# Performance work log

Measured on AMD Instinct MI355X. Metric: run time of the kernel, lower is better.

Reference implementation:

```python
import jax, jax.numpy as jnp
import numpy as np

THRESHOLD = 0.5
NEG_POS_RATIO = 3
ALPHA = 1.0
B, A, C, M = 128, 8732, 21, 8


def cxcy_to_xy(c):
    return jnp.concatenate([c[:, :2] - c[:, 2:] / 2.0, c[:, :2] + c[:, 2:] / 2.0], axis=1)


def cxcy_to_gcxgcy(cxcy, priors):
    g_cxcy = (cxcy[:, :2] - priors[:, :2]) / (priors[:, 2:] / 10.0)
    g_wh = jnp.log(cxcy[:, 2:] / priors[:, 2:]) * 5.0
    return jnp.concatenate([g_cxcy, g_wh], axis=1)


def find_jaccard_overlap(a, b):
    # a: [M,4] xy, b: [A,4] xy -> IoU [M,A]
    lt = jnp.maximum(a[:, None, :2], b[None, :, :2])
    rb = jnp.minimum(a[:, None, 2:], b[None, :, 2:])
    wh = jnp.clip(rb - lt, 0.0)
    inter = wh[..., 0] * wh[..., 1]
    area_a = (a[:, 2] - a[:, 0]) * (a[:, 3] - a[:, 1])
    area_b = (b[:, 2] - b[:, 0]) * (b[:, 3] - b[:, 1])
    return inter / (area_a[:, None] + area_b[None, :] - inter)


def setup_inputs() -> dict:
    key = jax.random.key(0)
    k1, k2, k3, k4, k5, k6 = jax.random.split(key, 6)
    predicted_locs = jax.random.normal(k1, (B, A, 4), dtype=jnp.float32)
    predicted_scores = jax.random.normal(k2, (B, A, C), dtype=jnp.float32)
    # ground-truth boxes in xy pixel coords within [0, 300], guaranteed x2>x1, y2>y1
    u = jax.random.uniform(k3, (B, M, 4), dtype=jnp.float32)
    x1y1 = u[..., :2] * 150.0
    x2y2 = x1y1 + u[..., 2:] * 140.0 + 10.0
    boxes = jnp.concatenate([x1y1, x2y2], axis=-1)
    labels = jax.random.randint(k4, (B, M), 1, C)  # 1..20, never background
    # anchor boxes in cxcy, w/h strictly positive
    cxcy = jax.random.uniform(k5, (A, 2), dtype=jnp.float32)
    wh = 0.05 + 0.95 * jax.random.uniform(k6, (A, 2), dtype=jnp.float32)
    anchor_boxes = jnp.concatenate([cxcy, wh], axis=1)
    return {"predicted_locs": predicted_locs, "predicted_scores": predicted_scores,
            "boxes": boxes, "labels": labels, "anchor_boxes": anchor_boxes}


def _match(boxes_i, labels_i, anchors_cxcy, anchors_xy):
    # boxes_i: [M,4] xy pixels, labels_i: [M]
    scaled = boxes_i / 300.0
    iou = find_jaccard_overlap(scaled, anchors_xy)            # [M, A]
    obj_for_anchor = jnp.argmax(iou, axis=0)                  # [A]
    iou_for_anchor = jnp.max(iou, axis=0)                     # [A]
    anchor_for_obj = jnp.argmax(iou, axis=1)                  # [M]
    obj_for_anchor = obj_for_anchor.at[anchor_for_obj].set(jnp.arange(M))
    iou_for_anchor = iou_for_anchor.at[anchor_for_obj].set(1.0)
    label_for_anchor = labels_i[obj_for_anchor]               # [A]
    label_for_anchor = jnp.where(iou_for_anchor < THRESHOLD, 0, label_for_anchor)
    true_locs = cxcy_to_gcxgcy(boxes_i[obj_for_anchor], anchors_cxcy)  # [A,4]
    return label_for_anchor, true_locs


def reference(predicted_locs, predicted_scores, boxes, labels, anchor_boxes):
    anchors_xy = cxcy_to_xy(anchor_boxes)
    true_classes, true_locs = jax.vmap(_match, in_axes=(0, 0, None, None))(
        boxes, labels, anchor_boxes, anchors_xy)              # [B,A], [B,A,4]

    pos = true_classes != 0                                   # [B,A]
    n_pos = pos.sum(axis=1)                                   # [B]
    n_pos_total = n_pos.sum()

    # L1Loss(mean) over positive anchors' 4 coords
    l1 = jnp.abs(predicted_locs - true_locs)                  # [B,A,4]
    loc_loss = (l1 * pos[..., None]).sum() / (n_pos_total.astype(jnp.float32) * 4.0)

    # per-anchor cross entropy
    logp = jax.nn.log_softmax(predicted_scores, axis=-1)      # [B,A,C]
    ce = -jnp.take_along_axis(logp, true_classes[..., None], axis=-1)[..., 0]  # [B,A]

    conf_pos = (ce * pos).sum()
    ce_neg = jnp.where(pos, 0.0, ce)
    ce_neg_sorted = -jnp.sort(-ce_neg, axis=1)                # descending per row
    ranks = jnp.arange(A)[None, :]
    hard = ranks < (NEG_POS_RATIO * n_pos)[:, None]
    conf_hard_neg = (ce_neg_sorted * hard).sum()

    conf_loss = (conf_hard_neg + conf_pos) / n_pos_total.astype(jnp.float32)
    return conf_loss + ALPHA * loc_loss
```

## Files before the change

### kernel.cpp

```cpp
#include <hip/hip_runtime.h>

constexpr int B = 128;
constexpr int A = 8732;
constexpr int C = 21;
constexpr int M = 8;


__global__ __launch_bounds__(1024) void k_match(
    const float* __restrict__ boxes,
    const int*   __restrict__ labels,
    const float* __restrict__ anchors,
    const float* __restrict__ plocs,
    int*         __restrict__ packed,
    int*         __restrict__ row_npos,
    float*       __restrict__ row_loc,
    float*       __restrict__ accf)
{
    __shared__ float         s_iou[A];
    __shared__ unsigned char s_obj[A];
    __shared__ float s_pv[M][16];
    __shared__ int   s_pi[M][16];
    __shared__ int   s_force[M];
    __shared__ int   s_c[16];
    __shared__ float s_l[16];
    __shared__ float s_box[M][4];
    __shared__ int   s_lab[M];

    const int b = blockIdx.x;
    const int t = threadIdx.x;
    const int lane = t & 63;
    const int wv   = t >> 6;

    if (t < M * 4) ((float*)s_box)[t] = boxes[b * M * 4 + t];
    if (t < M)     s_lab[t] = labels[b * M + t];
    __syncthreads();

    float bb[M][4], barea[M];
#pragma unroll
    for (int m = 0; m < M; m++) {
        bb[m][0] = s_box[m][0] / 300.f;
        bb[m][1] = s_box[m][1] / 300.f;
        bb[m][2] = s_box[m][2] / 300.f;
        bb[m][3] = s_box[m][3] / 300.f;
        barea[m] = (bb[m][2] - bb[m][0]) * (bb[m][3] - bb[m][1]);
    }

    float bestv[M];
    int   besti[M];
#pragma unroll
    for (int m = 0; m < M; m++) { bestv[m] = -1.f; besti[m] = 0; }

    const float4* anch4 = (const float4*)anchors;
    for (int a = t; a < A; a += 1024) {
        float4 an = anch4[a];
        float ax1 = an.x - an.z / 2.0f, ay1 = an.y - an.w / 2.0f;
        float ax2 = an.x + an.z / 2.0f, ay2 = an.y + an.w / 2.0f;
        float aarea = (ax2 - ax1) * (ay2 - ay1);

        float bmax = -1.f; int bm = 0;
#pragma unroll
        for (int m = 0; m < M; m++) {
            float lx = fmaxf(bb[m][0], ax1), ly = fmaxf(bb[m][1], ay1);
            float rx = fminf(bb[m][2], ax2), ry = fminf(bb[m][3], ay2);
            float iw = fmaxf(rx - lx, 0.f), ih = fmaxf(ry - ly, 0.f);
            float inter = iw * ih;
            float iou = inter / (barea[m] + aarea - inter);
            if (iou > bmax) { bmax = iou; bm = m; }
            if (iou > bestv[m]) { bestv[m] = iou; besti[m] = a; }
        }
        s_iou[a] = bmax;
        s_obj[a] = (unsigned char)bm;
    }

#pragma unroll
    for (int m = 0; m < M; m++) {
        float v = bestv[m]; int i = besti[m];
        for (int off = 32; off > 0; off >>= 1) {
            float ov = __shfl_down(v, off);
            int   oi = __shfl_down(i, off);
            if (ov > v || (ov == v && oi < i)) { v = ov; i = oi; }
        }
        if (lane == 0) { s_pv[m][wv] = v; s_pi[m][wv] = i; }
    }
    __syncthreads();

    if (t < M) {
        float bv = -1.f; int bi = 0x7fffffff;
#pragma unroll
        for (int w = 0; w < 16; w++) {
            float v = s_pv[t][w]; int i = s_pi[t][w];
            if (v > bv || (v == bv && i < bi)) { bv = v; bi = i; }
        }
        s_force[t] = bi;
    }
    __syncthreads();

    if (t == 0) {
        for (int m = 0; m < M; m++) {
            int a = s_force[m];
            s_obj[a] = (unsigned char)m;
            s_iou[a] = 1.0f;
        }
    }
    __syncthreads();

    int cnt = 0; float lloc = 0.f;
    for (int a = t; a < A; a += 1024) {
        int obj = s_obj[a];
        int lab = (s_iou[a] < 0.5f) ? 0 : s_lab[obj];
        packed[(size_t)b * A + a] = lab;
        if (lab != 0) {
            cnt++;
            float4 an = anch4[a];
            const float* bx = s_box[obj];
            float dx = (bx[0] - an.x) / (an.z / 10.f);
            float dy = (bx[1] - an.y) / (an.w / 10.f);
            float dw = logf(bx[2] / an.z) * 5.f;
            float dh = logf(bx[3] / an.w) * 5.f;
            float4 p = ((const float4*)plocs)[(size_t)b * A + a];
            lloc += fabsf(p.x - dx) + fabsf(p.y - dy) +
                    fabsf(p.z - dw) + fabsf(p.w - dh);
        }
    }
    for (int off = 32; off > 0; off >>= 1) {
        cnt  += __shfl_down(cnt, off);
        lloc += __shfl_down(lloc, off);
    }
    if (lane == 0) { s_c[wv] = cnt; s_l[wv] = lloc; }
    __syncthreads();
    if (t == 0) {
        int tc = 0; float tl = 0.f;
#pragma unroll
        for (int w = 0; w < 16; w++) { tc += s_c[w]; tl += s_l[w]; }
        row_npos[b] = tc;
        row_loc[b]  = tl;
        if (b == 0) accf[0] = 0.f;
    }
}

__global__ __launch_bounds__(256, 4) void k_ce(
    const float* __restrict__ pscores,
    int*         __restrict__ buf,
    float*       __restrict__ accf)
{
    const int tid = blockIdx.x * 256 + threadIdx.x;
    const int q = tid >> 1;
    const int h = tid & 1;
    const float4* sp = (const float4*)pscores + (size_t)q * 21;

    float4 r[11];
    if (h == 0) {
#pragma unroll
        for (int j = 0; j < 11; j++) r[j] = sp[j];
    } else {
#pragma unroll
        for (int j = 0; j < 10; j++) r[j] = sp[11 + j];
    }
    const int4 pk4 = ((const int4*)buf)[q];
    const int labs[4] = {pk4.x, pk4.y, pk4.z, pk4.w};

    float sum[4] = {0.f, 0.f, 0.f, 0.f};
    float sel[4] = {0.f, 0.f, 0.f, 0.f};

    if (h == 0) {
#pragma unroll
        for (int j = 0; j < 11; j++) {
            const float vv[4] = {r[j].x, r[j].y, r[j].z, r[j].w};
#pragma unroll
            for (int e = 0; e < 4; e++) {
                const int fi = j * 4 + e;
                const int al = fi / 21, c = fi % 21;
                sum[al] += __expf(vv[e]);
                if (c == labs[al]) sel[al] = vv[e];
            }
        }
    } else {
#pragma unroll
        for (int j = 0; j < 10; j++) {
            const float vv[4] = {r[j].x, r[j].y, r[j].z, r[j].w};
#pragma unroll
            for (int e = 0; e < 4; e++) {
                const int fi = 44 + j * 4 + e;
                const int al = fi / 21, c = fi % 21;
                sum[al] += __expf(vv[e]);
                if (c == labs[al]) sel[al] = vv[e];
            }
        }
    }
#pragma unroll
    for (int al = 0; al < 4; al++) {
        sum[al] += __shfl_xor(sum[al], 1);
        sel[al] += __shfl_xor(sel[al], 1);
    }

    float l_pos = 0.f;
    if (h == 0) {
        float4 cn;
        float* cnp = (float*)&cn;
#pragma unroll
        for (int al = 0; al < 4; al++) {
            float ce = __logf(sum[al]) - sel[al];
            ce = fmaxf(ce, 0.f);
            if (labs[al] != 0) { l_pos += ce; ce = 0.f; }
            cnp[al] = ce;
        }
        ((float4*)buf)[q] = cn;
    }
    for (int off = 32; off > 0; off >>= 1) l_pos += __shfl_down(l_pos, off);
    if ((threadIdx.x & 63) == 0 && l_pos != 0.f) atomicAdd(&accf[0], l_pos);
}

__global__ __launch_bounds__(1024) void k_topk(
    const float* __restrict__ ce_neg,
    const int*   __restrict__ row_npos,
    float*       __restrict__ row_hard)
{
    __shared__ unsigned vals[A];
    __shared__ unsigned s_u[16];
    __shared__ float    s_f[16];

    const int b = blockIdx.x;
    const int t = threadIdx.x;
    const int lane = t & 63;
    const int wv   = t >> 6;
    const int K = 3 * row_npos[b];
    const float* row = ce_neg + (size_t)b * A;

    {
        const uint4* r4 = (const uint4*)row;
        uint4* v4 = (uint4*)vals;
        for (int i = t; i < A / 4; i += 1024) v4[i] = r4[i];
    }
    __syncthreads();

    if (K <= 0) { if (t == 0) row_hard[b] = 0.f; return; }

    if (K >= A) {
        float s = 0.f;
        for (int i = t; i < A; i += 1024) s += __uint_as_float(vals[i]);
        for (int off = 32; off > 0; off >>= 1) s += __shfl_down(s, off);
        if (lane == 0) s_f[wv] = s;
        __syncthreads();
        if (t == 0) {
            float tot = 0.f;
#pragma unroll
            for (int w = 0; w < 16; w++) tot += s_f[w];
            row_hard[b] = tot;
        }
        return;
    }

    unsigned lo = 0u, hi = 0x7F800000u;
    while (lo < hi) {
        const unsigned mid = lo + ((hi - lo) >> 1);
        int cnt = 0;
        for (int i = t; i < A; i += 1024) cnt += (vals[i] > mid) ? 1 : 0;
        for (int off = 32; off > 0; off >>= 1) cnt += __shfl_down(cnt, off);
        if (lane == 0) s_u[wv] = (unsigned)cnt;
        __syncthreads();
        int tot = 0;
#pragma unroll
        for (int w = 0; w < 16; w++) tot += (int)s_u[w];
        if (tot < K) hi = mid; else lo = mid + 1;
        __syncthreads();
    }
    const unsigned tb = lo;

    float sg = 0.f; int cg = 0;
    for (int i = t; i < A; i += 1024) {
        unsigned v = vals[i];
        if (v > tb) { sg += __uint_as_float(v); cg++; }
    }
    for (int off = 32; off > 0; off >>= 1) {
        sg += __shfl_down(sg, off);
        cg += __shfl_down(cg, off);
    }
    if (lane == 0) { s_f[wv] = sg; s_u[wv] = (unsigned)cg; }
    __syncthreads();
    if (t == 0) {
        float tot = 0.f; int cnt = 0;
#pragma unroll
        for (int w = 0; w < 16; w++) { tot += s_f[w]; cnt += (int)s_u[w]; }
        row_hard[b] = tot + (float)(K - cnt) * __uint_as_float(tb);
    }
}

__global__ __launch_bounds__(128) void k_final(
    const float* __restrict__ accf,
    const int*   __restrict__ row_npos,
    const float* __restrict__ row_loc,
    const float* __restrict__ row_hard,
    float*       __restrict__ out)
{
    __shared__ int   s_n[2];
    __shared__ float s_l[2], s_h[2];
    const int t = threadIdx.x;
    const int lane = t & 63;
    const int wv = t >> 6;

    int np = row_npos[t];
    float lc = row_loc[t];
    float hd = row_hard[t];
    for (int off = 32; off > 0; off >>= 1) {
        np += __shfl_down(np, off);
        lc += __shfl_down(lc, off);
        hd += __shfl_down(hd, off);
    }
    if (lane == 0) { s_n[wv] = np; s_l[wv] = lc; s_h[wv] = hd; }
    __syncthreads();
    if (t == 0) {
        float n = (float)(s_n[0] + s_n[1]);
        float conf = (accf[0] + s_h[0] + s_h[1]) / n;
        float loc  = (s_l[0] + s_l[1]) / (n * 4.f);
        out[0] = conf + loc;
    }
}

extern "C" void kernel_launch(void* const* d_in, const int* in_sizes, int n_in,
                              void* d_out, int out_size, void* d_ws, size_t ws_size,
                              hipStream_t stream)
{
    const float* plocs   = (const float*)d_in[0];
    const float* pscores = (const float*)d_in[1];
    const float* boxes   = (const float*)d_in[2];
    const int*   labels  = (const int*)d_in[3];
    const float* anchors = (const float*)d_in[4];
    float*       out     = (float*)d_out;

    float* accf     = (float*)d_ws;
    int*   row_npos = (int*)d_ws + 8;
    float* row_loc  = (float*)d_ws + 136;
    float* row_hard = (float*)d_ws + 264;
    int*   buf      = (int*)d_ws + 392;

    k_match<<<B, 1024, 0, stream>>>(boxes, labels, anchors, plocs,
                                    buf, row_npos, row_loc, accf);
    k_ce<<<(B * A / 2) / 256, 256, 0, stream>>>(pscores, buf, accf);
    k_topk<<<B, 1024, 0, stream>>>((const float*)buf, row_npos, row_hard);
    k_final<<<1, 128, 0, stream>>>(accf, row_npos, row_loc, row_hard, out);
}
```

Baseline: 292.0 us.

## Stage CE scores through LDS, keep top-k row in registers, fuse final reduce

The cross-entropy kernel becomes a grid-stride loop in which each wave loads 64 anchors' scores with coalesced float4 reads into LDS, and each lane then handles one anchor. The top-k kernel keeps its row in registers instead of LDS, double-buffers the per-wave counts so each bisection step needs one barrier instead of two, and folds the final reduction into the last block through an atomic done counter. This removes one kernel launch and a round of LDS traffic and barriers. The cost is a threadfence/atomic handshake, plus reliance on k_match resetting the counter on every call.

Measured after the change: 319.1 us. +9.3%, slower.

```diff
diff --git a/kernel.cpp b/kernel.cpp
--- a/kernel.cpp
+++ b/kernel.cpp
@@ -14,7 +14,8 @@
     int*         __restrict__ packed,
     int*         __restrict__ row_npos,
     float*       __restrict__ row_loc,
-    float*       __restrict__ accf)
+    float*       __restrict__ accf,
+    int*         __restrict__ done)
 {
     __shared__ float         s_iou[A];
     __shared__ unsigned char s_obj[A];
@@ -134,90 +135,77 @@
         for (int w = 0; w < 16; w++) { tc += s_c[w]; tl += s_l[w]; }
         row_npos[b] = tc;
         row_loc[b]  = tl;
-        if (b == 0) accf[0] = 0.f;
+        if (b == 0) { accf[0] = 0.f; *done = 0; }
     }
 }
 
-__global__ __launch_bounds__(256, 4) void k_ce(
+__global__ __launch_bounds__(256) void k_ce(
     const float* __restrict__ pscores,
     int*         __restrict__ buf,
     float*       __restrict__ accf)
 {
-    const int tid = blockIdx.x * 256 + threadIdx.x;
-    const int q = tid >> 1;
-    const int h = tid & 1;
-    const float4* sp = (const float4*)pscores + (size_t)q * 21;
-
-    float4 r[11];
-    if (h == 0) {
-#pragma unroll
-        for (int j = 0; j < 11; j++) r[j] = sp[j];
-    } else {
-#pragma unroll
-        for (int j = 0; j < 10; j++) r[j] = sp[11 + j];
-    }
-    const int4 pk4 = ((const int4*)buf)[q];
-    const int labs[4] = {pk4.x, pk4.y, pk4.z, pk4.w};
-
-    float sum[4] = {0.f, 0.f, 0.f, 0.f};
-    float sel[4] = {0.f, 0.f, 0.f, 0.f};
-
-    if (h == 0) {
-#pragma unroll
-        for (int j = 0; j < 11; j++) {
-            const float vv[4] = {r[j].x, r[j].y, r[j].z, r[j].w};
-#pragma unroll
-            for (int e = 0; e < 4; e++) {
-                const int fi = j * 4 + e;
-                const int al = fi / 21, c = fi % 21;
-                sum[al] += __expf(vv[e]);
-                if (c == labs[al]) sel[al] = vv[e];
-            }
-        }
-    } else {
-#pragma unroll
-        for (int j = 0; j < 10; j++) {
-            const float vv[4] = {r[j].x, r[j].y, r[j].z, r[j].w};
-#pragma unroll
-            for (int e = 0; e < 4; e++) {
-                const int fi = 44 + j * 4 + e;
-                const int al = fi / 21, c = fi % 21;
-                sum[al] += __expf(vv[e]);
-                if (c == labs[al]) sel[al] = vv[e];
-            }
-        }
-    }
-#pragma unroll
-    for (int al = 0; al < 4; al++) {
-        sum[al] += __shfl_xor(sum[al], 1);
-        sel[al] += __shfl_xor(sel[al], 1);
-    }
-
-    float l_pos = 0.f;
-    if (h == 0) {
-        float4 cn;
-        float* cnp = (float*)&cn;
-#pragma unroll
-        for (int al = 0; al < 4; al++) {
-            float ce = __logf(sum[al]) - sel[al];
-            ce = fmaxf(ce, 0.f);
-            if (labs[al] != 0) { l_pos += ce; ce = 0.f; }
-            cnp[al] = ce;
-        }
-        ((float4*)buf)[q] = cn;
-    }
-    for (int off = 32; off > 0; off >>= 1) l_pos += __shfl_down(l_pos, off);
-    if ((threadIdx.x & 63) == 0 && l_pos != 0.f) atomicAdd(&accf[0], l_pos);
+    __shared__ float4 s_sc[4][336];
+    const int t    = threadIdx.x;
+    const int lane = t & 63;
+    const int wv   = t >> 6;
+    float4* lds4 = s_sc[wv];
+    const float* lds = (const float*)s_sc[wv];
+
+    const int gw = blockIdx.x * 4 + wv;
+    const int nw = gridDim.x * 4;
+    constexpr int NW = (B * A) / 64;
+
+    for (int wc = gw; wc < NW; wc += nw) {
+        const int base = wc * 64;
+        const float4* src = (const float4*)(pscores + (size_t)base * C);
+        float4 r0 = src[lane];
+        float4 r1 = src[lane + 64];
+        float4 r2 = src[lane + 128];
+        float4 r3 = src[lane + 192];
+        float4 r4 = src[lane + 256];
+        float4 r5;
+        if (lane < 16) r5 = src[lane + 320];
+        const int lab = buf[base + lane];
+
+        lds4[lane]       = r0;
+        lds4[lane + 64]  = r1;
+        lds4[lane + 128] = r2;
+        lds4[lane + 192] = r3;
+        lds4[lane + 256] = r4;
+        if (lane < 16) lds4[lane + 320] = r5;
+
+        const float* row = lds + lane * C;
+        float sum = 0.f, sel = 0.f;
+#pragma unroll
+        for (int c = 0; c < C; c++) {
+            float v = row[c];
+            sum += __expf(v);
+            if (c == lab) sel = v;
+        }
+        float ce = fmaxf(__logf(sum) - sel, 0.f);
+        float l_pos = 0.f;
+        if (lab != 0) { l_pos = ce; ce = 0.f; }
+        ((float*)buf)[base + lane] = ce;
+
+        for (int off = 32; off > 0; off >>= 1) l_pos += __shfl_down(l_pos, off);
+        if (lane == 0 && l_pos != 0.f) atomicAdd(&accf[0], l_pos);
+    }
 }
 
 __global__ __launch_bounds__(1024) void k_topk(
     const float* __restrict__ ce_neg,
     const int*   __restrict__ row_npos,
-    float*       __restrict__ row_hard)
+    const float* __restrict__ row_loc,
+    float*       __restrict__ row_hard,
+    const float* __restrict__ accf,
+    int*         __restrict__ done,
+    float*       __restrict__ out)
 {
-    __shared__ unsigned vals[A];
-    __shared__ unsigned s_u[16];
+    __shared__ unsigned s_u[2][16];
     __shared__ float    s_f[16];
+    __shared__ int      s_i[16];
+    __shared__ float    s_g[16];
+    __shared__ int      s_last;
 
     const int b = blockIdx.x;
     const int t = threadIdx.x;
@@ -226,93 +214,90 @@
     const int K = 3 * row_npos[b];
     const float* row = ce_neg + (size_t)b * A;
 
-    {
-        const uint4* r4 = (const uint4*)row;
-        uint4* v4 = (uint4*)vals;
-        for (int i = t; i < A / 4; i += 1024) v4[i] = r4[i];
-    }
-    __syncthreads();
-
-    if (K <= 0) { if (t == 0) row_hard[b] = 0.f; return; }
-
+    unsigned u[9];
+#pragma unroll
+    for (int k = 0; k < 9; k++) {
+        int i = t + k * 1024;
+        u[k] = (i < A) ? __float_as_uint(row[i]) : 0u;
+    }
+
+    float hard = 0.f;
     if (K >= A) {
         float s = 0.f;
-        for (int i = t; i < A; i += 1024) s += __uint_as_float(vals[i]);
+#pragma unroll
+        for (int k = 0; k < 9; k++) s += __uint_as_float(u[k]);
         for (int off = 32; off > 0; off >>= 1) s += __shfl_down(s, off);
         if (lane == 0) s_f[wv] = s;
         __syncthreads();
         if (t == 0) {
-            float tot = 0.f;
-#pragma unroll
-            for (int w = 0; w < 16; w++) tot += s_f[w];
-            row_hard[b] = tot;
-        }
-        return;
-    }
-
-    unsigned lo = 0u, hi = 0x7F800000u;
-    while (lo < hi) {
-        const unsigned mid = lo + ((hi - lo) >> 1);
-        int cnt = 0;
-        for (int i = t; i < A; i += 1024) cnt += (vals[i] > mid) ? 1 : 0;
-        for (int off = 32; off > 0; off >>= 1) cnt += __shfl_down(cnt, off);
-        if (lane == 0) s_u[wv] = (unsigned)cnt;
-        __syncthreads();
-        int tot = 0;
-#pragma unroll
-        for (int w = 0; w < 16; w++) tot += (int)s_u[w];
-        if (tot < K) hi = mid; else lo = mid + 1;
-        __syncthreads();
-    }
-    const unsigned tb = lo;
-
-    float sg = 0.f; int cg = 0;
-    for (int i = t; i < A; i += 1024) {
-        unsigned v = vals[i];
-        if (v > tb) { sg += __uint_as_float(v); cg++; }
-    }
-    for (int off = 32; off > 0; off >>= 1) {
-        sg += __shfl_down(sg, off);
-        cg += __shfl_down(cg, off);
-    }
-    if (lane == 0) { s_f[wv] = sg; s_u[wv] = (unsigned)cg; }
-    __syncthreads();
+#pragma unroll
+            for (int w = 0; w < 16; w++) hard += s_f[w];
+        }
+        __syncthreads();
+    } else if (K > 0) {
+        unsigned lo = 0u, hi = 0x7F800000u;
+        int it = 0;
+        while (lo < hi) {
+            const unsigned mid = lo + ((hi - lo) >> 1);
+            int cnt = 0;
+#pragma unroll
+            for (int k = 0; k < 9; k++) cnt += (u[k] > mid) ? 1 : 0;
+            for (int off = 32; off > 0; off >>= 1) cnt += __shfl_down(cnt, off);
+            if (lane == 0) s_u[it & 1][wv] = (unsigned)cnt;
+            __syncthreads();
+            int tot = 0;
+#pragma unroll
+            for (int w = 0; w < 16; w++) tot += (int)s_u[it & 1][w];
+            if (tot < K) hi = mid; else lo = mid + 1;
+            it++;
+        }
+        const unsigned tb = lo;
+
+        float sg = 0.f; int cg = 0;
+#pragma unroll
+        for (int k = 0; k < 9; k++) {
+            unsigned v = u[k];
+            if (v > tb) { sg += __uint_as_float(v); cg++; }
+        }
+        for (int off = 32; off > 0; off >>= 1) {
+            sg += __shfl_down(sg, off);
+            cg += __shfl_down(cg, off);
+        }
+        if (lane == 0) { s_f[wv] = sg; s_u[0][wv] = (unsigned)cg; }
+        __syncthreads();
+        if (t == 0) {
+            float tot = 0.f; int cnt = 0;
+#pragma unroll
+            for (int w = 0; w < 16; w++) { tot += s_f[w]; cnt += (int)s_u[0][w]; }
+            hard = tot + (float)(K - cnt) * __uint_as_float(tb);
+        }
+        __syncthreads();
+    }
+
     if (t == 0) {
-        float tot = 0.f; int cnt = 0;
-#pragma unroll
-        for (int w = 0; w < 16; w++) { tot += s_f[w]; cnt += (int)s_u[w]; }
-        row_hard[b] = tot + (float)(K - cnt) * __uint_as_float(tb);
-    }
-}
-
-__global__ __launch_bounds__(128) void k_final(
-    const float* __restrict__ accf,
-    const int*   __restrict__ row_npos,
-    const float* __restrict__ row_loc,
-    const float* __restrict__ row_hard,
-    float*       __restrict__ out)
-{
-    __shared__ int   s_n[2];
-    __shared__ float s_l[2], s_h[2];
-    const int t = threadIdx.x;
-    const int lane = t & 63;
-    const int wv = t >> 6;
-
-    int np = row_npos[t];
-    float lc = row_loc[t];
-    float hd = row_hard[t];
-    for (int off = 32; off > 0; off >>= 1) {
-        np += __shfl_down(np, off);
-        lc += __shfl_down(lc, off);
-        hd += __shfl_down(hd, off);
-    }
-    if (lane == 0) { s_n[wv] = np; s_l[wv] = lc; s_h[wv] = hd; }
-    __syncthreads();
-    if (t == 0) {
-        float n = (float)(s_n[0] + s_n[1]);
-        float conf = (accf[0] + s_h[0] + s_h[1]) / n;
-        float loc  = (s_l[0] + s_l[1]) / (n * 4.f);
-        out[0] = conf + loc;
+        row_hard[b] = hard;
+        __threadfence();
+        s_last = (atomicAdd(done, 1) == B - 1);
+    }
+    __syncthreads();
+
+    if (s_last) {
+        __threadfence();
+        int np = 0; float lc = 0.f, hd = 0.f;
+        if (t < B) { np = row_npos[t]; lc = row_loc[t]; hd = row_hard[t]; }
+        for (int off = 32; off > 0; off >>= 1) {
+            np += __shfl_down(np, off);
+            lc += __shfl_down(lc, off);
+            hd += __shfl_down(hd, off);
+        }
+        if (lane == 0) { s_i[wv] = np; s_f[wv] = lc; s_g[wv] = hd; }
+        __syncthreads();
+        if (t == 0) {
+            float n = (float)(s_i[0] + s_i[1]);
+            float conf = (accf[0] + s_g[0] + s_g[1]) / n;
+            float loc  = (s_f[0] + s_f[1]) / (n * 4.f);
+            out[0] = conf + loc;
+        }
     }
 }
 
@@ -328,14 +313,15 @@
     float*       out     = (float*)d_out;
 
     float* accf     = (float*)d_ws;
+    int*   done     = (int*)d_ws + 1;
     int*   row_npos = (int*)d_ws + 8;
     float* row_loc  = (float*)d_ws + 136;
     float* row_hard = (float*)d_ws + 264;
     int*   buf      = (int*)d_ws + 392;
 
     k_match<<<B, 1024, 0, stream>>>(boxes, labels, anchors, plocs,
-                                    buf, row_npos, row_loc, accf);
-    k_ce<<<(B * A / 2) / 256, 256, 0, stream>>>(pscores, buf, accf);
-    k_topk<<<B, 1024, 0, stream>>>((const float*)buf, row_npos, row_hard);
-    k_final<<<1, 128, 0, stream>>>(accf, row_npos, row_loc, row_hard, out);
+                                    buf, row_npos, row_loc, accf, done);
+    k_ce<<<1792, 256, 0, stream>>>(pscores, buf, accf);
+    k_topk<<<B, 1024, 0, stream>>>((const float*)buf, row_npos, row_loc,
+                                   row_hard, accf, done, out);
 }
```
